# Optimization experiments

Measured on AMD Instinct MI355X. Metric: run time of the kernel, lower is better.

The kernel has to match this reference:

```python
import jax, jax.numpy as jnp
import numpy as np

HIDDEN = 1024
HEADS = 16
HEAD_D = HIDDEN // HEADS
FILL = -10000.0


def setup_inputs() -> dict:
    key = jax.random.key(0)
    ks = jax.random.split(key, 5)
    scale = 1.0 / np.sqrt(HIDDEN)
    x = jax.random.normal(ks[0], (2, 2048, HIDDEN), dtype=jnp.float32)
    # nn.Linear weights stored as [in, out] (already transposed vs torch)
    W_qkv = jax.random.uniform(ks[1], (HIDDEN, 3 * HIDDEN), dtype=jnp.float32, minval=-scale, maxval=scale)
    b_qkv = jax.random.uniform(ks[2], (3 * HIDDEN,), dtype=jnp.float32, minval=-scale, maxval=scale)
    W_o = jax.random.uniform(ks[3], (HIDDEN, HIDDEN), dtype=jnp.float32, minval=-scale, maxval=scale)
    b_o = jax.random.uniform(ks[4], (HIDDEN,), dtype=jnp.float32, minval=-scale, maxval=scale)
    return {"x": x, "W_qkv": W_qkv, "b_qkv": b_qkv, "W_o": W_o, "b_o": b_o}


def reference(x, W_qkv, b_qkv, W_o, b_o):
    b, s, _ = x.shape
    qkv = x @ W_qkv + b_qkv                       # [b, s, 3*hidden]
    q, k, v = jnp.split(qkv, 3, axis=-1)
    # [b, s, hidden] -> [b, h, s, d]
    def to_heads(t):
        return t.reshape(b, s, HEADS, HEAD_D).transpose(0, 2, 1, 3)
    q, k, v = to_heads(q), to_heads(k), to_heads(v)
    logits = jnp.einsum('bhqd,bhkd->bhqk', q, k) / np.sqrt(HEAD_D).astype(np.float32)
    # Faithful to the original: tril, then fill anything equal to 0 (incl.
    # genuine zeros) with the masked_logit_fill value.
    logits_tril = jnp.tril(logits)
    logits_masked = jnp.where(logits_tril == 0.0, jnp.float32(FILL), logits_tril)
    probs = jax.nn.softmax(logits_masked, axis=-1)
    pre_o = jnp.einsum('bhqk,bhkd->bhqd', probs, v)    # [b, h, s, d]
    pre_o = pre_o.transpose(0, 2, 1, 3).reshape(b, s, HIDDEN)
    return pre_o @ W_o + b_o
```

## Files before the change

kernel.cpp:

```cpp
#include <hip/hip_runtime.h>

typedef __attribute__((ext_vector_type(8))) short short8;
typedef __attribute__((ext_vector_type(4))) short short4b;
typedef __attribute__((ext_vector_type(4))) float f32x4;

static __device__ __forceinline__ short f2bf(float f) {
    unsigned u = __builtin_bit_cast(unsigned, f);
    u += 0x7FFFu + ((u >> 16) & 1u);
    return (short)(u >> 16);
}

static __device__ __forceinline__ void g2l16(const void* g, void* l) {
    __builtin_amdgcn_global_load_lds(
        (const __attribute__((address_space(1))) unsigned*)g,
        (__attribute__((address_space(3))) unsigned*)l, 16, 0, 0);
}

__global__ void convert_x(const float* __restrict__ x, short* __restrict__ xb, int n4) {
    int i = blockIdx.x * blockDim.x + threadIdx.x;
    if (i >= n4) return;
    f32x4 v = *(const f32x4*)&x[(long)i * 4];
    short4b o;
    #pragma unroll
    for (int j = 0; j < 4; ++j) o[j] = f2bf(v[j]);
    *(short4b*)&xb[(long)i * 4] = o;
}

__global__ void transpose_conv(const float* __restrict__ W, short* __restrict__ Wt,
                               int K, int N) {
    __shared__ float lds[64][65];
    const int t = threadIdx.x;
    const int n0 = blockIdx.x * 64, k0 = blockIdx.y * 64;
    const int rr = t >> 4, q4 = (t & 15) * 4;
    #pragma unroll
    for (int p = 0; p < 4; ++p) {
        int k = rr + p * 16;
        f32x4 v = *(const f32x4*)&W[(long)(k0 + k) * N + n0 + q4];
        #pragma unroll
        for (int j = 0; j < 4; ++j) lds[k][q4 + j] = v[j];
    }
    __syncthreads();
    #pragma unroll
    for (int p = 0; p < 4; ++p) {
        int nloc = rr + p * 16;
        short4b o;
        #pragma unroll
        for (int j = 0; j < 4; ++j) o[j] = f2bf(lds[q4 + j][nloc]);
        *(short4b*)&Wt[(long)(n0 + nloc) * K + k0 + q4] = o;
    }
}

template<int F32OUT, int QSCALE>
__global__ __launch_bounds__(256, 2)
void gemm_bt(const short* __restrict__ A, const short* __restrict__ Bt,
             const float* __restrict__ bias, void* __restrict__ C,
             int M, int N, int K) {
    __shared__ short lA[128 * 32];
    __shared__ short lB[128 * 32];
    const int t = threadIdx.x;
    const int lane = t & 63, w = t >> 6;
    const int m0 = blockIdx.y * 128, n0 = blockIdx.x * 128;
    const int lr = lane & 15, lk = lane >> 4;
    const int wr = w >> 1, wc = w & 1;

    f32x4 acc[4][4];
    #pragma unroll
    for (int i = 0; i < 4; ++i)
        #pragma unroll
        for (int j = 0; j < 4; ++j)
            #pragma unroll
            for (int e = 0; e < 4; ++e) acc[i][j][e] = 0.0f;

    const int nsteps = K >> 5;
    for (int kt = 0; kt < nsteps; ++kt) {
        const int kb = kt * 32;
        #pragma unroll
        for (int c = 0; c < 2; ++c) {
            int off  = c * 4096 + w * 1024;
            int offl = off + lane * 16;
            int ra = offl >> 6;
            int ca = (offl & 63) >> 1;
            g2l16(A  + (long)(m0 + ra) * K + kb + ca, (short*)lA + (off >> 1));
            g2l16(Bt + (long)(n0 + ra) * K + kb + ca, (short*)lB + (off >> 1));
        }
        __syncthreads();
        short8 af[4], bf[4];
        #pragma unroll
        for (int m = 0; m < 4; ++m)
            af[m] = *(const short8*)&lA[(wr * 64 + m * 16 + lr) * 32 + lk * 8];
        #pragma unroll
        for (int n = 0; n < 4; ++n)
            bf[n] = *(const short8*)&lB[(wc * 64 + n * 16 + lr) * 32 + lk * 8];
        #pragma unroll
        for (int m = 0; m < 4; ++m)
            #pragma unroll
            for (int n = 0; n < 4; ++n)
                acc[m][n] = __builtin_amdgcn_mfma_f32_16x16x32_bf16(af[m], bf[n], acc[m][n], 0, 0, 0);
        __syncthreads();
    }

    #pragma unroll
    for (int n = 0; n < 4; ++n) {
        int col = n0 + wc * 64 + n * 16 + lr;
        float bb = bias[col];
        float sc = (QSCALE && col < 1024) ? 0.125f : 1.0f;
        #pragma unroll
        for (int m = 0; m < 4; ++m) {
            int rowb = m0 + wr * 64 + m * 16 + lk * 4;
            #pragma unroll
            for (int r = 0; r < 4; ++r) {
                float v = (acc[m][n][r] + bb) * sc;
                if (F32OUT) ((float*)C)[(long)(rowb + r) * N + col] = v;
                else        ((short*)C)[(long)(rowb + r) * N + col] = f2bf(v);
            }
        }
    }
}

__global__ void build_vt(const short* __restrict__ qkv, short* __restrict__ vt) {
    __shared__ short lds[64][72];
    const int t = threadIdx.x;
    const int st = blockIdx.x, bh = blockIdx.y;
    const int b = bh >> 4, h = bh & 15;
    const int s0 = st * 64;
    const int sr = t >> 3, c8 = (t & 7) * 8;
    #pragma unroll
    for (int p = 0; p < 2; ++p) {
        int s = sr + p * 32;
        short8 v = *(const short8*)&qkv[(long)(b * 2048 + s0 + s) * 3072 + 2048 + h * 64 + c8];
        *(short8*)&lds[s][c8] = v;
    }
    __syncthreads();
    #pragma unroll
    for (int p = 0; p < 2; ++p) {
        int d = sr + p * 32;
        short8 v;
        #pragma unroll
        for (int j = 0; j < 8; ++j) v[j] = lds[c8 + j][d];
        *(short8*)&vt[(long)(bh * 64 + d) * 2048 + s0 + c8] = v;
    }
}

__device__ const signed char rQ[44]  = {19,18,17,16,15, 31,31,30, 14,30,29,29,28,
                                        13,28,27,27,26, 12,26,25,25,24, 11,24,23,23,22,
                                        10,22,21,21,20, 9,20, 8,7,6,5,4,3,2,1,0};
__device__ const signed char rK0[44] = { 0, 0, 0, 0, 0,  0,16,15,  0, 0, 0,15,14,
                                          0, 0, 0,14,13,  0, 0, 0,13,12,  0, 0, 0,12,11,
                                          0, 0, 0,11,10,  0, 0, 0,0,0,0,0,0,0,0,0};
__device__ const signed char rK1[44] = {20,19,18,17,16, 16,32,31, 15,15,15,30,29,
                                        14,14,14,28,27, 13,13,13,26,25, 12,12,12,24,23,
                                        11,11,11,22,21, 10,10, 9,8,7,6,5,4,3,2,1};
__device__ const signed char rHf[44] = {-1,-1,-1,-1,-1,  0, 1, 1, -1, 0, 0, 1, 1,
                                        -1, 0, 0, 1, 1, -1, 0, 0, 1, 1, -1, 0, 0, 1, 1,
                                        -1, 0, 0, 1, 1, -1, 0, -1,-1,-1,-1,-1,-1,-1,-1,-1};

__global__ __launch_bounds__(256, 4)
void attn_kernel(const short* __restrict__ qkv, const short* __restrict__ vt,
                 short* __restrict__ pre_o, float* __restrict__ pO,
                 float* __restrict__ pML) {
    __shared__ short lK[2][64 * 64];
    __shared__ short lV[2][64 * 64];
    __shared__ short lP[4][16 * 64];
    const int t = threadIdx.x, lane = t & 63, w = t >> 6;
    const int lr = lane & 15, lk = lane >> 4;
    const int bh = blockIdx.x, rank = blockIdx.y;
    const int b = bh >> 4, h = bh & 15;

    const int Q    = rQ[rank];
    const int kt0  = rK0[rank];
    const int kt1  = rK1[rank];
    const int half = rHf[rank];
    const int q0 = Q * 64;

    int soff[2], sRow[2], sCol[2];
    #pragma unroll
    for (int c = 0; c < 2; ++c) {
        int off  = c * 4096 + w * 1024;
        int offl = off + lane * 16;
        int r    = offl >> 7;
        soff[c]  = off >> 1;
        sRow[c]  = r;
        sCol[c]  = (((offl >> 4) & 7) ^ (r & 7)) * 8;
    }

    short8 aq[2];
    #pragma unroll
    for (int dk = 0; dk < 2; ++dk)
        aq[dk] = *(const short8*)&qkv[(long)(b * 2048 + q0 + w * 16 + lr) * 3072
                                      + h * 64 + dk * 32 + lk * 8];

    f32x4 accO[4];
    #pragma unroll
    for (int n = 0; n < 4; ++n)
        #pragma unroll
        for (int e = 0; e < 4; ++e) accO[n][e] = 0.0f;
    float mst[4], lst[4];
    #pragma unroll
    for (int r = 0; r < 4; ++r) { mst[r] = -1e30f; lst[r] = 0.0f; }

    #pragma unroll
    for (int c = 0; c < 2; ++c) {
        g2l16(qkv + (long)(b * 2048 + kt0 * 64 + sRow[c]) * 3072 + 1024 + h * 64 + sCol[c],
              &lK[0][soff[c]]);
        g2l16(vt + (long)(bh * 64 + sRow[c]) * 2048 + kt0 * 64 + sCol[c],
              &lV[0][soff[c]]);
    }
    __syncthreads();

    #pragma unroll 1
    for (int kt = kt0; kt < kt1; ++kt) {
        const int cur = (kt - kt0) & 1;
        if (kt + 1 < kt1) {
            #pragma unroll
            for (int c = 0; c < 2; ++c) {
                g2l16(qkv + (long)(b * 2048 + (kt + 1) * 64 + sRow[c]) * 3072
                          + 1024 + h * 64 + sCol[c],
                      &lK[cur ^ 1][soff[c]]);
                g2l16(vt + (long)(bh * 64 + sRow[c]) * 2048 + (kt + 1) * 64 + sCol[c],
                      &lV[cur ^ 1][soff[c]]);
            }
        }

        f32x4 accS[4];
        #pragma unroll
        for (int n = 0; n < 4; ++n) {
            #pragma unroll
            for (int e = 0; e < 4; ++e) accS[n][e] = 0.0f;
            #pragma unroll
            for (int dk = 0; dk < 2; ++dk) {
                short8 bk = *(const short8*)((const char*)&lK[cur][0]
                             + (n * 16 + lr) * 128 + (((dk * 4 + lk) ^ (lr & 7)) << 4));
                accS[n] = __builtin_amdgcn_mfma_f32_16x16x32_bf16(aq[dk], bk, accS[n], 0, 0, 0);
            }
        }

        const bool diag = (kt == Q);
        #pragma unroll
        for (int r = 0; r < 4; ++r) {
            int qrow = q0 + w * 16 + lk * 4 + r;
            float sv[4];
            #pragma unroll
            for (int n = 0; n < 4; ++n) {
                float s = accS[n][r];
                if (diag) {
                    int key = kt * 64 + n * 16 + lr;
                    if (key > qrow || s == 0.0f) s = -10000.0f;
                } else {
                    if (s == 0.0f) s = -10000.0f;
                }
                sv[n] = s;
            }
            float mx = fmaxf(fmaxf(sv[0], sv[1]), fmaxf(sv[2], sv[3]));
            mx = fmaxf(mx, __shfl_xor(mx, 1));
            mx = fmaxf(mx, __shfl_xor(mx, 2));
            mx = fmaxf(mx, __shfl_xor(mx, 4));
            mx = fmaxf(mx, __shfl_xor(mx, 8));
            float mnew = fmaxf(mst[r], mx);
            float corr = __expf(mst[r] - mnew);
            mst[r] = mnew;
            float rs = 0.0f;
            #pragma unroll
            for (int n = 0; n < 4; ++n) { float p = __expf(sv[n] - mnew); sv[n] = p; rs += p; }
            rs += __shfl_xor(rs, 1);
            rs += __shfl_xor(rs, 2);
            rs += __shfl_xor(rs, 4);
            rs += __shfl_xor(rs, 8);
            lst[r] = lst[r] * corr + rs;
            #pragma unroll
            for (int n = 0; n < 4; ++n) accO[n][r] *= corr;
            int prr = lk * 4 + r;
            int swz = (prr & 7) << 4;
            #pragma unroll
            for (int n = 0; n < 4; ++n) {
                int pc = n * 16 + lr;
                *(short*)((char*)&lP[w][0] + prr * 128 + ((pc * 2) ^ swz)) = f2bf(sv[n]);
            }
        }

        short8 ap[2];
        #pragma unroll
        for (int kk = 0; kk < 2; ++kk)
            ap[kk] = *(const short8*)((const char*)&lP[w][0] + lr * 128
                                      + (((kk * 4 + lk) ^ (lr & 7)) << 4));
        #pragma unroll
        for (int n = 0; n < 4; ++n)
            #pragma unroll
            for (int kk = 0; kk < 2; ++kk) {
                short8 bv = *(const short8*)((const char*)&lV[cur][0]
                             + (n * 16 + lr) * 128 + (((kk * 4 + lk) ^ (lr & 7)) << 4));
                accO[n] = __builtin_amdgcn_mfma_f32_16x16x32_bf16(ap[kk], bv, accO[n], 0, 0, 0);
            }

        __syncthreads();
    }

    if (half < 0) {
        #pragma unroll
        for (int r = 0; r < 4; ++r) {
            int qrow = q0 + w * 16 + lk * 4 + r;
            float inv = 1.0f / lst[r];
            #pragma unroll
            for (int n = 0; n < 4; ++n)
                pre_o[(long)(b * 2048 + qrow) * 1024 + h * 64 + n * 16 + lr] =
                    f2bf(accO[n][r] * inv);
        }
    } else {
        const int g2 = ((Q - 20) * 32 + bh) * 2 + half;
        float* U  = pO  + (long)g2 * 4096;
        float* ML = pML + (long)g2 * 128;
        #pragma unroll
        for (int r = 0; r < 4; ++r) {
            int row = w * 16 + lk * 4 + r;
            #pragma unroll
            for (int n = 0; n < 4; ++n)
                U[row * 64 + n * 16 + lr] = accO[n][r];
            if (lr == 0) { ML[row * 2] = mst[r]; ML[row * 2 + 1] = lst[r]; }
        }
    }
}

__global__ __launch_bounds__(256)
void attn_combine(const float* __restrict__ pO, const float* __restrict__ pML,
                  short* __restrict__ pre_o) {
    const int g = blockIdx.x;
    const int Q = 20 + (g >> 5), bh = g & 31, b = bh >> 4, h = bh & 15;
    const int t = threadIdx.x;
    const int row = t >> 2, d0 = (t & 3) * 16;
    const float* ML0 = pML + ((long)(g * 2 + 0)) * 128 + row * 2;
    const float* ML1 = pML + ((long)(g * 2 + 1)) * 128 + row * 2;
    float m0 = ML0[0], l0 = ML0[1], m1 = ML1[0], l1 = ML1[1];
    float m = fmaxf(m0, m1);
    float e0 = __expf(m0 - m), e1 = __expf(m1 - m);
    float inv = 1.0f / (l0 * e0 + l1 * e1);
    const float* U0 = pO + ((long)(g * 2 + 0)) * 4096 + row * 64 + d0;
    const float* U1 = pO + ((long)(g * 2 + 1)) * 4096 + row * 64 + d0;
    long out = ((long)(b * 2048 + Q * 64 + row)) * 1024 + h * 64 + d0;
    #pragma unroll
    for (int j = 0; j < 16; j += 4) {
        f32x4 a = *(const f32x4*)&U0[j];
        f32x4 c = *(const f32x4*)&U1[j];
        #pragma unroll
        for (int e = 0; e < 4; ++e)
            pre_o[out + j + e] = f2bf((a[e] * e0 + c[e] * e1) * inv);
    }
}

extern "C" void kernel_launch(void* const* d_in, const int* in_sizes, int n_in,
                              void* d_out, int out_size, void* d_ws, size_t ws_size,
                              hipStream_t stream) {
    const float* x    = (const float*)d_in[0];
    const float* Wqkv = (const float*)d_in[1];
    const float* bqkv = (const float*)d_in[2];
    const float* Wo   = (const float*)d_in[3];
    const float* bo   = (const float*)d_in[4];
    float* out = (float*)d_out;

    char* ws = (char*)d_ws;
    short* xb    = (short*)(ws);
    short* wqkvT = (short*)(ws + (8L  << 20));
    short* woT   = (short*)(ws + (14L << 20));
    short* qkv   = (short*)(ws + (16L << 20));
    short* vt    = (short*)(ws + (40L << 20));
    short* preo  = (short*)(ws + (48L << 20));
    float* pO    = (float*)(ws);
    float* pML   = (float*)(ws + 12779520L);

    convert_x<<<4096, 256, 0, stream>>>(x, xb, 4096 * 1024 / 4);
    transpose_conv<<<dim3(48, 16), 256, 0, stream>>>(Wqkv, wqkvT, 1024, 3072);
    transpose_conv<<<dim3(16, 16), 256, 0, stream>>>(Wo, woT, 1024, 1024);
    gemm_bt<0, 1><<<dim3(24, 32), 256, 0, stream>>>(xb, wqkvT, bqkv, qkv, 4096, 3072, 1024);
    build_vt<<<dim3(32, 32), 256, 0, stream>>>(qkv, vt);
    attn_kernel<<<dim3(32, 44), 256, 0, stream>>>(qkv, vt, preo, pO, pML);
    attn_combine<<<384, 256, 0, stream>>>(pO, pML, preo);
    gemm_bt<1, 0><<<dim3(8, 32), 256, 0, stream>>>(preo, woT, bo, out, 4096, 1024, 1024);
}
```

Before: 227.5 us.

## Load K and V fragments directly from global memory instead of LDS staging

Removes the double-buffered LDS staging of K and V tiles and the per-iteration block barrier. Each wave now reads its MFMA B-operand fragments straight from global memory (through the caches), and the occupancy hint is raised from 4 to 6 blocks per CU. This cuts LDS use and synchronisation, but each of the four waves now fetches the same K/V tile separately, and the loads are no longer prefetched one tile ahead, which exposes global-memory latency in the inner loop.

```diff
diff --git a/kernel.cpp b/kernel.cpp
--- a/kernel.cpp
+++ b/kernel.cpp
@@ -154,12 +154,10 @@
                                         -1, 0, 0, 1, 1, -1, 0, 0, 1, 1, -1, 0, 0, 1, 1,
                                         -1, 0, 0, 1, 1, -1, 0, -1,-1,-1,-1,-1,-1,-1,-1,-1};
 
-__global__ __launch_bounds__(256, 4)
+__global__ __launch_bounds__(256, 6)
 void attn_kernel(const short* __restrict__ qkv, const short* __restrict__ vt,
                  short* __restrict__ pre_o, float* __restrict__ pO,
                  float* __restrict__ pML) {
-    __shared__ short lK[2][64 * 64];
-    __shared__ short lV[2][64 * 64];
     __shared__ short lP[4][16 * 64];
     const int t = threadIdx.x, lane = t & 63, w = t >> 6;
     const int lr = lane & 15, lk = lane >> 4;
@@ -172,23 +170,15 @@
     const int half = rHf[rank];
     const int q0 = Q * 64;
 
-    int soff[2], sRow[2], sCol[2];
-    #pragma unroll
-    for (int c = 0; c < 2; ++c) {
-        int off  = c * 4096 + w * 1024;
-        int offl = off + lane * 16;
-        int r    = offl >> 7;
-        soff[c]  = off >> 1;
-        sRow[c]  = r;
-        sCol[c]  = (((offl >> 4) & 7) ^ (r & 7)) * 8;
-    }
-
     short8 aq[2];
     #pragma unroll
     for (int dk = 0; dk < 2; ++dk)
         aq[dk] = *(const short8*)&qkv[(long)(b * 2048 + q0 + w * 16 + lr) * 3072
                                       + h * 64 + dk * 32 + lk * 8];
 
+    const short* Kbase = qkv + (long)(b * 2048 + lr) * 3072 + 1024 + h * 64 + lk * 8;
+    const short* Vbase = vt + (long)(bh * 64 + lr) * 2048 + lk * 8;
+
     f32x4 accO[4];
     #pragma unroll
     for (int n = 0; n < 4; ++n)
@@ -198,29 +188,8 @@
     #pragma unroll
     for (int r = 0; r < 4; ++r) { mst[r] = -1e30f; lst[r] = 0.0f; }
 
-    #pragma unroll
-    for (int c = 0; c < 2; ++c) {
-        g2l16(qkv + (long)(b * 2048 + kt0 * 64 + sRow[c]) * 3072 + 1024 + h * 64 + sCol[c],
-              &lK[0][soff[c]]);
-        g2l16(vt + (long)(bh * 64 + sRow[c]) * 2048 + kt0 * 64 + sCol[c],
-              &lV[0][soff[c]]);
-    }
-    __syncthreads();
-
     #pragma unroll 1
     for (int kt = kt0; kt < kt1; ++kt) {
-        const int cur = (kt - kt0) & 1;
-        if (kt + 1 < kt1) {
-            #pragma unroll
-            for (int c = 0; c < 2; ++c) {
-                g2l16(qkv + (long)(b * 2048 + (kt + 1) * 64 + sRow[c]) * 3072
-                          + 1024 + h * 64 + sCol[c],
-                      &lK[cur ^ 1][soff[c]]);
-                g2l16(vt + (long)(bh * 64 + sRow[c]) * 2048 + (kt + 1) * 64 + sCol[c],
-                      &lV[cur ^ 1][soff[c]]);
-            }
-        }
-
         f32x4 accS[4];
         #pragma unroll
         for (int n = 0; n < 4; ++n) {
@@ -228,8 +197,7 @@
             for (int e = 0; e < 4; ++e) accS[n][e] = 0.0f;
             #pragma unroll
             for (int dk = 0; dk < 2; ++dk) {
-                short8 bk = *(const short8*)((const char*)&lK[cur][0]
-                             + (n * 16 + lr) * 128 + (((dk * 4 + lk) ^ (lr & 7)) << 4));
+                short8 bk = *(const short8*)(Kbase + (long)(kt * 64 + n * 16) * 3072 + dk * 32);
                 accS[n] = __builtin_amdgcn_mfma_f32_16x16x32_bf16(aq[dk], bk, accS[n], 0, 0, 0);
             }
         }
@@ -286,12 +254,9 @@
         for (int n = 0; n < 4; ++n)
             #pragma unroll
             for (int kk = 0; kk < 2; ++kk) {
-                short8 bv = *(const short8*)((const char*)&lV[cur][0]
-                             + (n * 16 + lr) * 128 + (((kk * 4 + lk) ^ (lr & 7)) << 4));
+                short8 bv = *(const short8*)(Vbase + (long)(n * 16) * 2048 + kt * 64 + kk * 32);
                 accO[n] = __builtin_amdgcn_mfma_f32_16x16x32_bf16(ap[kk], bv, accO[n], 0, 0, 0);
             }
-
-        __syncthreads();
     }
 
     if (half < 0) {
```

Measured after the change: 307.8 us. 35.3% more time.
